# Performance work log

Hardware: AMD Instinct MI355X
Metric: run time of the kernel (lower is better)

The kernel has to match this reference:

```python
import jax, jax.numpy as jnp
import numpy as np

EMBED = 100
BATCH = 4096
NUM_NEG = 256
U, P, W, RP, B, C = 30000, 50000, 100000, 50000, 5000, 1000


def _tab(k, v, e=EMBED):
    r = 0.5 / e
    w = jax.random.uniform(k, (v + 1, e), minval=-r, maxval=r, dtype=jnp.float32)
    return w.at[-1].set(0.0)  # padding row is zeros, as in torch code


def setup_inputs() -> dict:
    key = jax.random.key(0)
    ks = jax.random.split(key, 10)
    inp = {
        'user_emb': _tab(ks[0], U),
        'product_emb': _tab(ks[1], P),
        'word_emb': _tab(ks[2], W),
        'brand_emb': _tab(ks[3], B),
        'category_emb': _tab(ks[4], C),
        'rproduct_emb': _tab(ks[5], RP),
        'rel_vecs': jax.random.uniform(ks[6], (8, EMBED), minval=-0.5 / EMBED, maxval=0.5 / EMBED, dtype=jnp.float32),
        'purchase_bias': jnp.zeros((P + 1,), jnp.float32),
        'mentions_bias': jnp.zeros((W + 1,), jnp.float32),
        'describe_bias': jnp.zeros((W + 1,), jnp.float32),
        'produced_bias': jnp.zeros((B + 1,), jnp.float32),
        'belongs_bias': jnp.zeros((C + 1,), jnp.float32),
        'also_bought_bias': jnp.zeros((RP + 1,), jnp.float32),
        'also_viewed_bias': jnp.zeros((RP + 1,), jnp.float32),
        'together_bias': jnp.zeros((RP + 1,), jnp.float32),
    }
    # batch_idxs columns: (u, p, w, b, c, rp1, rp2, rp3), each in its own vocab range
    col_max = [U, P, W, B, C, RP, RP, RP]
    cols = [jax.random.randint(jax.random.fold_in(ks[7], i), (BATCH,), 0, m) for i, m in enumerate(col_max)]
    inp['batch_idxs'] = jnp.stack(cols, axis=1)
    # deterministic stand-in for torch.multinomial negative sampling, one row per relation
    neg_max = [P, W, W, B, C, RP, RP, RP]
    negs = [jax.random.randint(jax.random.fold_in(ks[8], i), (NUM_NEG,), 0, m) for i, m in enumerate(neg_max)]
    inp['neg_idxs'] = jnp.stack(negs, axis=0)
    return inp


def _neg_loss(head_tab, tail_tab, rvec, bias_tab, h, t, n):
    hv = head_tab[h]                      # [B,E] gather
    ex = hv + rvec                        # [B,E]
    tv = tail_tab[t]                      # [B,E]
    bias = bias_tab[t]                    # [B]
    pos = jnp.sum(ex * tv, axis=-1) + bias  # bmm([B,1,E],[B,E,1]) == rowwise dot
    nv = tail_tab[n]                      # [N,E]
    neg = jnp.einsum('be,ne->bn', ex, nv) + bias[:, None]  # [B,N]
    pos_loss = -jax.nn.log_sigmoid(pos)   # == -log(sigmoid(pos)), stable
    neg_loss = -jax.nn.log_sigmoid(-neg).sum(axis=1)
    return (pos_loss + neg_loss).mean()


def reference(batch_idxs, neg_idxs, user_emb, product_emb, word_emb, brand_emb,
              category_emb, rproduct_emb, rel_vecs, purchase_bias, mentions_bias,
              describe_bias, produced_bias, belongs_bias, also_bought_bias,
              also_viewed_bias, together_bias):
    # (head_tab, tail_tab, bias_tab, head_col, tail_col) per relation, in original order
    rels = [
        (user_emb, product_emb, purchase_bias, 0, 1),
        (user_emb, word_emb, mentions_bias, 0, 2),
        (product_emb, word_emb, describe_bias, 1, 2),
        (product_emb, brand_emb, produced_bias, 1, 3),
        (product_emb, category_emb, belongs_bias, 1, 4),
        (product_emb, rproduct_emb, also_bought_bias, 1, 5),
        (product_emb, rproduct_emb, also_viewed_bias, 1, 6),
        (product_emb, rproduct_emb, together_bias, 1, 7),
    ]
    loss = jnp.float32(0.0)
    for r, (ht, tt, bt, hc, tc) in enumerate(rels):
        loss = loss + _neg_loss(ht, tt, rel_vecs[r], bt,
                                batch_idxs[:, hc], batch_idxs[:, tc], neg_idxs[r])
    return loss
```

## Files before the change

kernel.cpp:

```cpp
#include <hip/hip_runtime.h>


#define EMBED   100
#define BATCH   4096
#define NUM_NEG 256
#define BM      64
#define BN      128
#define PITCH   136

typedef __attribute__((ext_vector_type(8))) short s8;
typedef __attribute__((ext_vector_type(4))) short s4;
typedef __attribute__((ext_vector_type(4))) float f4;

struct RelP {
    const float* head;
    const float* tail;
    const float* bias;
    int hc, tc;
};

struct Params {
    RelP rel[8];
    const float* rel_vecs;
    const int*   batch_idxs;
    const int*   neg_idxs;
    float*       out;
};

__device__ __forceinline__ float softplus_f(float x) {
    float e = __expf(-fabsf(x));
    return fmaxf(x, 0.0f) + __logf(1.0f + e);
}

__device__ __forceinline__ unsigned short bf16_rne(float f) {
    unsigned u = __float_as_uint(f);
    u += 0x7FFFu + ((u >> 16) & 1u);
    return (unsigned short)(u >> 16);
}

__device__ __forceinline__ float bf16_to_f(short s) {
    return __uint_as_float(((unsigned)(unsigned short)s) << 16);
}

__launch_bounds__(256, 4)
__global__ void ke_prep(Params p, short* aws, short* bws) {
    const int id  = blockIdx.x * 256 + threadIdx.x;
    const bool isA = id < 32768;
    const int r = isA ? (id >> 12) : ((id - 32768) >> 8);
    const RelP rp = p.rel[r];

    const float* src;
    unsigned short extra;
    short* dst;
    if (isA) {
        const int row = id & 4095;
        const int h  = p.batch_idxs[row * 8 + rp.hc];
        const int ti = p.batch_idxs[row * 8 + rp.tc];
        src   = rp.head + (size_t)h * EMBED;
        extra = bf16_rne(rp.bias[ti]);
        dst   = aws + (size_t)id * PITCH;
    } else {
        const int j = id - 32768;
        const int n = p.neg_idxs[(j >> 8) * NUM_NEG + (j & 255)];
        src   = rp.tail + (size_t)n * EMBED;
        extra = 0x3F80;
        dst   = bws + (size_t)j * PITCH;
    }

    const float4* s4p = (const float4*)src;
    const float4* rv4 = (const float4*)(p.rel_vecs + r * EMBED);

#pragma unroll
    for (int j = 0; j < 12; ++j) {
        float4 f0 = s4p[2 * j];
        float4 f1 = s4p[2 * j + 1];
        if (isA) {
            const float4 a = rv4[2 * j];
            const float4 b = rv4[2 * j + 1];
            f0.x += a.x; f0.y += a.y; f0.z += a.z; f0.w += a.w;
            f1.x += b.x; f1.y += b.y; f1.z += b.z; f1.w += b.w;
        }
        s8 v = { (short)bf16_rne(f0.x), (short)bf16_rne(f0.y),
                 (short)bf16_rne(f0.z), (short)bf16_rne(f0.w),
                 (short)bf16_rne(f1.x), (short)bf16_rne(f1.y),
                 (short)bf16_rne(f1.z), (short)bf16_rne(f1.w) };
        *(s8*)(dst + 8 * j) = v;
    }
    {
        float4 f = s4p[24];
        if (isA) {
            const float4 a = rv4[24];
            f.x += a.x; f.y += a.y; f.z += a.z; f.w += a.w;
        }
        s4 v = { (short)bf16_rne(f.x), (short)bf16_rne(f.y),
                 (short)bf16_rne(f.z), (short)bf16_rne(f.w) };
        *(s4*)(dst + 96) = v;
    }
    {
        s4 v = { (short)extra, 0, 0, 0 };
        *(s4*)(dst + 100) = v;
        s8 z = { 0,0,0,0,0,0,0,0 };
#pragma unroll
        for (int j = 0; j < 4; ++j)
            *(s8*)(dst + 104 + 8 * j) = z;
    }
}

__launch_bounds__(256, 3)
__global__ void ke_main(Params p, const short* aws, const short* bws) {
    const int bid = blockIdx.x;
    const int r   = bid & 7;
    const int rb  = (bid >> 3) & 63;
    const int nb  = bid >> 9;
    const int tid = threadIdx.x;

    __shared__ __align__(16) short As[BM * PITCH];
    __shared__ __align__(16) short Bs[BN * PITCH];

    const RelP rp = p.rel[r];

    {
        const s8* asrc = (const s8*)(aws + (size_t)(r * 4096 + rb * BM) * PITCH);
        s8* adst = (s8*)As;
#pragma unroll
        for (int j = 0; j < 4; ++j)
            adst[tid + 256 * j] = asrc[tid + 256 * j];
        if (tid < 64) adst[1024 + tid] = asrc[1024 + tid];

        const s8* bsrc = (const s8*)(bws + (size_t)(r * NUM_NEG + nb * BN) * PITCH);
        s8* bdst = (s8*)Bs;
#pragma unroll
        for (int j = 0; j < 8; ++j)
            bdst[tid + 256 * j] = bsrc[tid + 256 * j];
        if (tid < 128) bdst[2048 + tid] = bsrc[2048 + tid];
    }

    const bool doPos = (nb == 0) && (tid >= 192);
    const float* ptail = rp.tail;
    float pbias = 0.0f;
    if (doPos) {
        const int prow = rb * BM + (tid - 192);
        const int pt = p.batch_idxs[prow * 8 + rp.tc];
        ptail = rp.tail + (size_t)pt * EMBED;
        pbias = rp.bias[pt];
    }

    __syncthreads();

    const int wave = tid >> 6;
    const int lane = tid & 63;
    const int li   = lane & 15;
    const int q    = lane >> 4;
    const int wm   = wave & 1;
    const int wn   = wave >> 1;

    f4 acc[2][4];
#pragma unroll
    for (int i = 0; i < 2; ++i)
#pragma unroll
        for (int j = 0; j < 4; ++j)
            acc[i][j] = (f4){0.f, 0.f, 0.f, 0.f};

    const short* Abase = As + (wm * 32 + li) * PITCH + q * 8;
    const short* Bbase = Bs + (wn * 64 + li) * PITCH + q * 8;

#pragma unroll
    for (int s = 0; s < 4; ++s) {
        const s8 a0 = *(const s8*)(Abase +  0 * PITCH + s * 32);
        const s8 a1 = *(const s8*)(Abase + 16 * PITCH + s * 32);
        const s8 b0 = *(const s8*)(Bbase +  0 * PITCH + s * 32);
        const s8 b1 = *(const s8*)(Bbase + 16 * PITCH + s * 32);
        const s8 b2 = *(const s8*)(Bbase + 32 * PITCH + s * 32);
        const s8 b3 = *(const s8*)(Bbase + 48 * PITCH + s * 32);
        acc[0][0] = __builtin_amdgcn_mfma_f32_16x16x32_bf16(a0, b0, acc[0][0], 0, 0, 0);
        acc[0][1] = __builtin_amdgcn_mfma_f32_16x16x32_bf16(a0, b1, acc[0][1], 0, 0, 0);
        acc[0][2] = __builtin_amdgcn_mfma_f32_16x16x32_bf16(a0, b2, acc[0][2], 0, 0, 0);
        acc[0][3] = __builtin_amdgcn_mfma_f32_16x16x32_bf16(a0, b3, acc[0][3], 0, 0, 0);
        acc[1][0] = __builtin_amdgcn_mfma_f32_16x16x32_bf16(a1, b0, acc[1][0], 0, 0, 0);
        acc[1][1] = __builtin_amdgcn_mfma_f32_16x16x32_bf16(a1, b1, acc[1][1], 0, 0, 0);
        acc[1][2] = __builtin_amdgcn_mfma_f32_16x16x32_bf16(a1, b2, acc[1][2], 0, 0, 0);
        acc[1][3] = __builtin_amdgcn_mfma_f32_16x16x32_bf16(a1, b3, acc[1][3], 0, 0, 0);
    }

    float local = 0.0f;
#pragma unroll
    for (int i = 0; i < 2; ++i)
#pragma unroll
        for (int j = 0; j < 4; ++j) {
            local += softplus_f(acc[i][j].x);
            local += softplus_f(acc[i][j].y);
            local += softplus_f(acc[i][j].z);
            local += softplus_f(acc[i][j].w);
        }

    if (doPos) {
        const short* exr = As + (tid - 192) * PITCH;
        const float4* tv = (const float4*)ptail;
        float d0 = 0.f, d1 = 0.f, d2 = 0.f, d3 = 0.f;
#pragma unroll
        for (int j = 0; j < 25; ++j) {
            const s4 e = *(const s4*)(exr + 4 * j);
            const float4 v = tv[j];
            d0 = fmaf(bf16_to_f(e.x), v.x, d0);
            d1 = fmaf(bf16_to_f(e.y), v.y, d1);
            d2 = fmaf(bf16_to_f(e.z), v.z, d2);
            d3 = fmaf(bf16_to_f(e.w), v.w, d3);
        }
        const float pos = ((d0 + d1) + (d2 + d3)) + pbias;
        local += softplus_f(-pos);
    }

#pragma unroll
    for (int off = 32; off > 0; off >>= 1)
        local += __shfl_down(local, off, 64);

    __syncthreads();
    float* wsum = (float*)Bs;
    if (lane == 0) wsum[wave] = local;
    __syncthreads();
    if (tid == 0) {
        const float s = (wsum[0] + wsum[1]) + (wsum[2] + wsum[3]);
        atomicAdd(p.out, s * (1.0f / BATCH));
    }
}

extern "C" void kernel_launch(void* const* d_in, const int* in_sizes, int n_in,
                              void* d_out, int out_size, void* d_ws, size_t ws_size,
                              hipStream_t stream) {
    const float* user  = (const float*)d_in[0];
    const float* prod  = (const float*)d_in[1];
    const float* word  = (const float*)d_in[2];
    const float* brand = (const float*)d_in[3];
    const float* cat   = (const float*)d_in[4];
    const float* rprod = (const float*)d_in[5];

    Params p;
    p.rel_vecs   = (const float*)d_in[6];
    p.batch_idxs = (const int*)d_in[15];
    p.neg_idxs   = (const int*)d_in[16];
    p.out        = (float*)d_out;

    p.rel[0] = {user, prod,  (const float*)d_in[7],  0, 1};
    p.rel[1] = {user, word,  (const float*)d_in[8],  0, 2};
    p.rel[2] = {prod, word,  (const float*)d_in[9],  1, 2};
    p.rel[3] = {prod, brand, (const float*)d_in[10], 1, 3};
    p.rel[4] = {prod, cat,   (const float*)d_in[11], 1, 4};
    p.rel[5] = {prod, rprod, (const float*)d_in[12], 1, 5};
    p.rel[6] = {prod, rprod, (const float*)d_in[13], 1, 6};
    p.rel[7] = {prod, rprod, (const float*)d_in[14], 1, 7};

    short* aws = (short*)d_ws;
    short* bws = aws + (size_t)32768 * PITCH;

    hipMemsetAsync(d_out, 0, sizeof(float), stream);
    ke_prep<<<136, 256, 0, stream>>>(p, aws, bws);
    ke_main<<<1024, 256, 0, stream>>>(p, aws, bws);
}
```

Measured before the change: 169.0 us.

## Split prep rows across 8 threads and move positive loss into prep

The prep kernel now assigns each embedding row to 8 threads instead of one, so the gathers and bf16 conversion use many more threads and make more coalesced requests. The positive-pair dot product and its softplus move from the main GEMM kernel into prep, computed in fp32 from the gathered head and tail rows. This removes the serial per-thread positive-loss tail from the main kernel's last wave. The cost is extra atomics on shared memory and on the global output from 1024 prep blocks.

```diff
diff --git a/kernel.cpp b/kernel.cpp
--- a/kernel.cpp
+++ b/kernel.cpp
@@ -38,71 +38,97 @@
     return (unsigned short)(u >> 16);
 }
 
-__device__ __forceinline__ float bf16_to_f(short s) {
-    return __uint_as_float(((unsigned)(unsigned short)s) << 16);
-}
-
-__launch_bounds__(256, 4)
+__device__ __forceinline__ s8 pack8(float4 f0, float4 f1) {
+    s8 v = { (short)bf16_rne(f0.x), (short)bf16_rne(f0.y),
+             (short)bf16_rne(f0.z), (short)bf16_rne(f0.w),
+             (short)bf16_rne(f1.x), (short)bf16_rne(f1.y),
+             (short)bf16_rne(f1.z), (short)bf16_rne(f1.w) };
+    return v;
+}
+
+__launch_bounds__(256, 8)
 __global__ void ke_prep(Params p, short* aws, short* bws) {
-    const int id  = blockIdx.x * 256 + threadIdx.x;
-    const bool isA = id < 32768;
-    const int r = isA ? (id >> 12) : ((id - 32768) >> 8);
-    const RelP rp = p.rel[r];
-
-    const float* src;
-    unsigned short extra;
-    short* dst;
-    if (isA) {
-        const int row = id & 4095;
-        const int h  = p.batch_idxs[row * 8 + rp.hc];
-        const int ti = p.batch_idxs[row * 8 + rp.tc];
-        src   = rp.head + (size_t)h * EMBED;
-        extra = bf16_rne(rp.bias[ti]);
-        dst   = aws + (size_t)id * PITCH;
+    const int blk = blockIdx.x;
+    const int tid = threadIdx.x;
+    const int sub = tid & 7;
+
+    if (blk < 1024) {
+        __shared__ float psum;
+        if (tid == 0) psum = 0.0f;
+        __syncthreads();
+
+        const int row  = blk * 32 + (tid >> 3);
+        const int r    = row >> 12;
+        const int brow = row & 4095;
+        const RelP rp = p.rel[r];
+        const int h = p.batch_idxs[brow * 8 + rp.hc];
+        const int t = p.batch_idxs[brow * 8 + rp.tc];
+        const float4* hp = (const float4*)(rp.head + (size_t)h * EMBED);
+        const float4* tp = (const float4*)(rp.tail + (size_t)t * EMBED);
+        const float4* rv = (const float4*)(p.rel_vecs + r * EMBED);
+        short* dst = aws + (size_t)row * PITCH;
+
+        float partial = 0.0f;
+        if (sub < 6) {
+            const int b4 = sub * 4;
+            float4 e0 = hp[b4 + 0], e1 = hp[b4 + 1], e2 = hp[b4 + 2], e3 = hp[b4 + 3];
+            const float4 r0 = rv[b4 + 0], r1 = rv[b4 + 1], r2 = rv[b4 + 2], r3 = rv[b4 + 3];
+            e0.x += r0.x; e0.y += r0.y; e0.z += r0.z; e0.w += r0.w;
+            e1.x += r1.x; e1.y += r1.y; e1.z += r1.z; e1.w += r1.w;
+            e2.x += r2.x; e2.y += r2.y; e2.z += r2.z; e2.w += r2.w;
+            e3.x += r3.x; e3.y += r3.y; e3.z += r3.z; e3.w += r3.w;
+            *(s8*)(dst + 16 * sub)     = pack8(e0, e1);
+            *(s8*)(dst + 16 * sub + 8) = pack8(e2, e3);
+            const float4 t0 = tp[b4 + 0], t1 = tp[b4 + 1], t2 = tp[b4 + 2], t3 = tp[b4 + 3];
+            partial = e0.x*t0.x + e0.y*t0.y + e0.z*t0.z + e0.w*t0.w
+                    + e1.x*t1.x + e1.y*t1.y + e1.z*t1.z + e1.w*t1.w
+                    + e2.x*t2.x + e2.y*t2.y + e2.z*t2.z + e2.w*t2.w
+                    + e3.x*t3.x + e3.y*t3.y + e3.z*t3.z + e3.w*t3.w;
+        } else if (sub == 6) {
+            float4 e = hp[24];
+            const float4 r0 = rv[24];
+            e.x += r0.x; e.y += r0.y; e.z += r0.z; e.w += r0.w;
+            const float bias = rp.bias[t];
+            s8 v = { (short)bf16_rne(e.x), (short)bf16_rne(e.y),
+                     (short)bf16_rne(e.z), (short)bf16_rne(e.w),
+                     (short)bf16_rne(bias), 0, 0, 0 };
+            *(s8*)(dst + 96) = v;
+            const float4 t0 = tp[24];
+            partial = e.x*t0.x + e.y*t0.y + e.z*t0.z + e.w*t0.w + bias;
+        } else {
+            s8 z = {0,0,0,0,0,0,0,0};
+            *(s8*)(dst + 104) = z;
+            *(s8*)(dst + 120) = z;
+        }
+
+        partial += __shfl_down(partial, 4, 8);
+        partial += __shfl_down(partial, 2, 8);
+        partial += __shfl_down(partial, 1, 8);
+        if (sub == 0) atomicAdd(&psum, softplus_f(-partial));
+        __syncthreads();
+        if (tid == 0) atomicAdd(p.out, psum * (1.0f / BATCH));
     } else {
-        const int j = id - 32768;
-        const int n = p.neg_idxs[(j >> 8) * NUM_NEG + (j & 255)];
-        src   = rp.tail + (size_t)n * EMBED;
-        extra = 0x3F80;
-        dst   = bws + (size_t)j * PITCH;
-    }
-
-    const float4* s4p = (const float4*)src;
-    const float4* rv4 = (const float4*)(p.rel_vecs + r * EMBED);
-
-#pragma unroll
-    for (int j = 0; j < 12; ++j) {
-        float4 f0 = s4p[2 * j];
-        float4 f1 = s4p[2 * j + 1];
-        if (isA) {
-            const float4 a = rv4[2 * j];
-            const float4 b = rv4[2 * j + 1];
-            f0.x += a.x; f0.y += a.y; f0.z += a.z; f0.w += a.w;
-            f1.x += b.x; f1.y += b.y; f1.z += b.z; f1.w += b.w;
+        const int row = (blk - 1024) * 32 + (tid >> 3);
+        const int r   = row >> 8;
+        const int n   = p.neg_idxs[r * NUM_NEG + (row & 255)];
+        const float4* sp = (const float4*)(p.rel[r].tail + (size_t)n * EMBED);
+        short* dst = bws + (size_t)row * PITCH;
+
+        if (sub < 6) {
+            const int b4 = sub * 4;
+            *(s8*)(dst + 16 * sub)     = pack8(sp[b4 + 0], sp[b4 + 1]);
+            *(s8*)(dst + 16 * sub + 8) = pack8(sp[b4 + 2], sp[b4 + 3]);
+        } else if (sub == 6) {
+            const float4 f = sp[24];
+            s8 v = { (short)bf16_rne(f.x), (short)bf16_rne(f.y),
+                     (short)bf16_rne(f.z), (short)bf16_rne(f.w),
+                     (short)0x3F80, 0, 0, 0 };
+            *(s8*)(dst + 96) = v;
+        } else {
+            s8 z = {0,0,0,0,0,0,0,0};
+            *(s8*)(dst + 104) = z;
+            *(s8*)(dst + 120) = z;
         }
-        s8 v = { (short)bf16_rne(f0.x), (short)bf16_rne(f0.y),
-                 (short)bf16_rne(f0.z), (short)bf16_rne(f0.w),
-                 (short)bf16_rne(f1.x), (short)bf16_rne(f1.y),
-                 (short)bf16_rne(f1.z), (short)bf16_rne(f1.w) };
-        *(s8*)(dst + 8 * j) = v;
-    }
-    {
-        float4 f = s4p[24];
-        if (isA) {
-            const float4 a = rv4[24];
-            f.x += a.x; f.y += a.y; f.z += a.z; f.w += a.w;
-        }
-        s4 v = { (short)bf16_rne(f.x), (short)bf16_rne(f.y),
-                 (short)bf16_rne(f.z), (short)bf16_rne(f.w) };
-        *(s4*)(dst + 96) = v;
-    }
-    {
-        s4 v = { (short)extra, 0, 0, 0 };
-        *(s4*)(dst + 100) = v;
-        s8 z = { 0,0,0,0,0,0,0,0 };
-#pragma unroll
-        for (int j = 0; j < 4; ++j)
-            *(s8*)(dst + 104 + 8 * j) = z;
     }
 }
 
@@ -117,8 +143,6 @@
     __shared__ __align__(16) short As[BM * PITCH];
     __shared__ __align__(16) short Bs[BN * PITCH];
 
-    const RelP rp = p.rel[r];
-
     {
         const s8* asrc = (const s8*)(aws + (size_t)(r * 4096 + rb * BM) * PITCH);
         s8* adst = (s8*)As;
@@ -134,17 +158,6 @@
             bdst[tid + 256 * j] = bsrc[tid + 256 * j];
         if (tid < 128) bdst[2048 + tid] = bsrc[2048 + tid];
     }
-
-    const bool doPos = (nb == 0) && (tid >= 192);
-    const float* ptail = rp.tail;
-    float pbias = 0.0f;
-    if (doPos) {
-        const int prow = rb * BM + (tid - 192);
-        const int pt = p.batch_idxs[prow * 8 + rp.tc];
-        ptail = rp.tail + (size_t)pt * EMBED;
-        pbias = rp.bias[pt];
-    }
-
     __syncthreads();
 
     const int wave = tid >> 6;
@@ -193,23 +206,6 @@
             local += softplus_f(acc[i][j].w);
         }
 
-    if (doPos) {
-        const short* exr = As + (tid - 192) * PITCH;
-        const float4* tv = (const float4*)ptail;
-        float d0 = 0.f, d1 = 0.f, d2 = 0.f, d3 = 0.f;
-#pragma unroll
-        for (int j = 0; j < 25; ++j) {
-            const s4 e = *(const s4*)(exr + 4 * j);
-            const float4 v = tv[j];
-            d0 = fmaf(bf16_to_f(e.x), v.x, d0);
-            d1 = fmaf(bf16_to_f(e.y), v.y, d1);
-            d2 = fmaf(bf16_to_f(e.z), v.z, d2);
-            d3 = fmaf(bf16_to_f(e.w), v.w, d3);
-        }
-        const float pos = ((d0 + d1) + (d2 + d3)) + pbias;
-        local += softplus_f(-pos);
-    }
-
 #pragma unroll
     for (int off = 32; off > 0; off >>= 1)
         local += __shfl_down(local, off, 64);
@@ -253,6 +249,6 @@
     short* bws = aws + (size_t)32768 * PITCH;
 
     hipMemsetAsync(d_out, 0, sizeof(float), stream);
-    ke_prep<<<136, 256, 0, stream>>>(p, aws, bws);
+    ke_prep<<<1088, 256, 0, stream>>>(p, aws, bws);
     ke_main<<<1024, 256, 0, stream>>>(p, aws, bws);
 }
```

Result: no change. 170.0 us (+0.5%).
